# Kernel optimization log

Hardware: AMD Instinct MI355X
Metric: run time of the kernel (lower is better)

The kernel has to match this reference:

```python
import jax, jax.numpy as jnp
import numpy as np

TOPK = 7  # hard-coded k in cal_high_score_instance_mask
EPS_DICE = 1e-8


def setup_inputs() -> dict:
    key = jax.random.key(0)
    k1, k2, k3, k4 = jax.random.split(key, 4)
    b, n, v, h, w = 4, 16, 32, 160, 160
    pred_mask = jax.random.normal(k1, (b, 1, h, w), dtype=jnp.float32)
    encode_feat = jax.random.normal(k2, (b, v, h, w), dtype=jnp.float32)
    gt_instances = (jax.random.uniform(k3, (b, n, h, w)) > 0.8).astype(jnp.float32)
    # validity mask over instance slots
    gt_index_mask = jax.random.randint(k4, (b, n), 0, 2).astype(jnp.int32)
    return {
        "pred_mask": pred_mask,
        "encode_feat": encode_feat,
        "gt_instances": gt_instances,
        "gt_index_mask": gt_index_mask,
    }


def reference(pred_mask, encode_feat, gt_instances, gt_index_mask):
    b, v, h, w = encode_feat.shape
    n = gt_instances.shape[1]
    hw = h * w
    feat = encode_feat.reshape(b, v, hw)          # b, v, hw
    gt = gt_instances.reshape(b, n, hw)           # b, n, hw
    valid = gt_index_mask.astype(feat.dtype)      # b, n  (0/1)

    # ---- get_mean_embedding_vector: masked mean of embedding per instance
    pix = jnp.clip(gt.sum(-1), 1.0)               # b, n
    mean_emb = jnp.einsum('bvp,bnp->bnv', feat, gt) / pix[..., None]

    # ---- cal_high_score_instance_mask: topk over masked score map, gather embeddings
    pre_regions = pred_mask.reshape(b, 1, hw) * gt             # b, n, hw
    _wvals, idx = jax.lax.top_k(pre_regions, TOPK)              # b, n, k
    idx_flat = idx.reshape(b, n * TOPK)                         # b, n*k
    # gather embedding vectors at topk pixel locations -> b, n*k, v
    idx_feat_th = jnp.take_along_axis(feat, idx_flat[:, None, :], axis=2)
    idx_feat_th = jnp.transpose(idx_feat_th, (0, 2, 1))

    # ---- get_isntance_mask: embedding-vector x feature-map matmuls
    inst_masks = jnp.einsum('bkv,bvp->bkp', idx_feat_th, feat)  # b, n*k, hw
    mean_masks = jnp.einsum('bnv,bvp->bnp', mean_emb, feat)     # b, n, hw

    # ---- w_dice_loss on mean-embedding masks (valid instances only)
    p_mean = jax.nn.sigmoid(mean_masks)
    denom_mean = jnp.clip((p_mean ** 2).sum(-1) + (gt ** 2).sum(-1), EPS_DICE)
    dice_mean = 1.0 - 2.0 * (gt * p_mean).sum(-1) / denom_mean  # b, n
    mean_inst_loss = (dice_mean * valid).sum()

    # ---- w_dice_loss on topk-instance masks (target expanded over k)
    p_k = jax.nn.sigmoid(inst_masks.reshape(b, n, TOPK, hw))
    t_k = gt[:, :, None, :]                                     # b, n, 1, hw
    denom_k = jnp.clip((p_k ** 2).sum(-1) + (t_k ** 2).sum(-1), EPS_DICE)
    dice_k = 1.0 - 2.0 * (t_k * p_k).sum(-1) / denom_k          # b, n, k
    inst_loss = (dice_k * valid[..., None]).sum()

    # ---- l2_loss: masked squared distance of per-pixel embedding to instance mean
    diff = (feat[:, None, :, :] - mean_emb[..., None]) * gt[:, :, None, :]  # b, n, v, hw
    l2 = (diff ** 2).sum(-1) / pix[..., None]                   # b, n, v
    embedding_l2_loss = (l2.sum(-1) * valid).sum()

    return jnp.stack([mean_inst_loss, inst_loss, embedding_l2_loss])
```

## Files before the change

### kernel.cpp

```cpp
#include <hip/hip_runtime.h>
#include <cstdint>
#include <cstddef>

#define B 4
#define N 16
#define V 32
#define HW 25600
#define TOPK 7
#define NSLB 5
#define NCA 200
#define NCC 400

__device__ __forceinline__ bool better(float av, int ai, float bv, int bi) {
    return (av > bv) || (av == bv && ai < bi);
}


__device__ __forceinline__ void kTop_body(
    int slab, int tid,
    const float* __restrict__ pred, const float* __restrict__ gt,
    float* __restrict__ cand_val, int* __restrict__ cand_idx,
    float* __restrict__ cnt_part,
    float* rwv, int* rwi, float* csum) {
    int bn = slab / NSLB, sl = slab % NSLB;
    int b = bn >> 4;
    int lane = tid & 63, wave = tid >> 6;
    int base = sl * 5120;

    const float* gtrow = gt + (size_t)bn * HW + base;
    const float* pr = pred + (size_t)b * HW + base;

    float tv[TOPK]; int ti[TOPK];
#pragma unroll
    for (int j = 0; j < TOPK; ++j) { tv[j] = -INFINITY; ti[j] = 0x7fffffff; }
    float cnt = 0.f;

#pragma unroll
    for (int it = 0; it < 5; ++it) {
        int p = it * 1024 + tid * 4;
        float4 g4 = *reinterpret_cast<const float4*>(gtrow + p);
        float4 p4 = *reinterpret_cast<const float4*>(pr + p);
        cnt += g4.x + g4.y + g4.z + g4.w;
        float ca[4] = { p4.x * g4.x, p4.y * g4.y, p4.z * g4.z, p4.w * g4.w };
#pragma unroll
        for (int j = 0; j < 4; ++j) {
            float c = ca[j]; int pi = base + p + j;
            if (better(c, pi, tv[TOPK - 1], ti[TOPK - 1])) {
                tv[TOPK - 1] = c; ti[TOPK - 1] = pi;
#pragma unroll
                for (int q = TOPK - 2; q >= 0; --q) {
                    if (better(tv[q + 1], ti[q + 1], tv[q], ti[q])) {
                        float fv = tv[q]; int fi = ti[q];
                        tv[q] = tv[q + 1]; ti[q] = ti[q + 1];
                        tv[q + 1] = fv; ti[q + 1] = fi;
                    }
                }
            }
        }
    }

#pragma unroll
    for (int off = 32; off > 0; off >>= 1) cnt += __shfl_down(cnt, off);
    if (lane == 0) csum[wave] = cnt;
    __syncthreads();
    if (tid == 0) cnt_part[slab] = csum[0] + csum[1] + csum[2] + csum[3];

    int cbase = slab * TOPK;
    for (int r = 0; r < TOPK; ++r) {
        float bv = tv[0]; int bi = ti[0];
#pragma unroll
        for (int m = 1; m <= 32; m <<= 1) {
            float ov = __shfl_xor(bv, m);
            int oi = __shfl_xor(bi, m);
            if (better(ov, oi, bv, bi)) { bv = ov; bi = oi; }
        }
        if (lane == 0) { rwv[wave] = bv; rwi[wave] = bi; }
        __syncthreads();
        float fv = rwv[0]; int fi = rwi[0];
#pragma unroll
        for (int w = 1; w < 4; ++w)
            if (better(rwv[w], rwi[w], fv, fi)) { fv = rwv[w]; fi = rwi[w]; }
        if (ti[0] == fi) {
#pragma unroll
            for (int q = 0; q < TOPK - 1; ++q) { tv[q] = tv[q + 1]; ti[q] = ti[q + 1]; }
            tv[TOPK - 1] = -INFINITY; ti[TOPK - 1] = 0x7fffffff;
        }
        if (tid == 0) { cand_val[cbase + r] = fv; cand_idx[cbase + r] = fi; }
        __syncthreads();
    }
}

__device__ __forceinline__ void kA_body(
    int w, int tid,
    const float* __restrict__ feat, const float* __restrict__ gt,
    float* __restrict__ ms_part, float* __restrict__ s2_part) {
    int xcd = w & 7;
    int b = xcd >> 1;
    int ch = (w >> 3) * 2 + (xcd & 1);
    int c0 = ch * 128;
    int ng = tid >> 6, vg = (tid >> 3) & 7, pg = tid & 7;

    const float* gb = gt + (size_t)(b * N + ng * 4) * HW + c0 + pg * 4;
    const float* fb = feat + (size_t)(b * V + vg * 4) * HW + c0 + pg * 4;

    float acc[4][4];
#pragma unroll
    for (int i = 0; i < 4; ++i)
#pragma unroll
        for (int j = 0; j < 4; ++j) acc[i][j] = 0.f;
    float s2a[4] = { 0.f, 0.f, 0.f, 0.f };

#pragma unroll
    for (int q = 0; q < 4; ++q) {
        int p = q * 32;
        float4 g4[4], f4[4];
#pragma unroll
        for (int i = 0; i < 4; ++i)
            g4[i] = *reinterpret_cast<const float4*>(gb + (size_t)i * HW + p);
#pragma unroll
        for (int j = 0; j < 4; ++j)
            f4[j] = *reinterpret_cast<const float4*>(fb + (size_t)j * HW + p);
        float ffx = 0.f, ffy = 0.f, ffz = 0.f, ffw = 0.f;
#pragma unroll
        for (int j = 0; j < 4; ++j) {
            ffx = fmaf(f4[j].x, f4[j].x, ffx);
            ffy = fmaf(f4[j].y, f4[j].y, ffy);
            ffz = fmaf(f4[j].z, f4[j].z, ffz);
            ffw = fmaf(f4[j].w, f4[j].w, ffw);
        }
#pragma unroll
        for (int i = 0; i < 4; ++i) {
#pragma unroll
            for (int j = 0; j < 4; ++j) {
                acc[i][j] = fmaf(g4[i].x, f4[j].x, acc[i][j]);
                acc[i][j] = fmaf(g4[i].y, f4[j].y, acc[i][j]);
                acc[i][j] = fmaf(g4[i].z, f4[j].z, acc[i][j]);
                acc[i][j] = fmaf(g4[i].w, f4[j].w, acc[i][j]);
            }
            s2a[i] = fmaf(g4[i].x, ffx, s2a[i]);
            s2a[i] = fmaf(g4[i].y, ffy, s2a[i]);
            s2a[i] = fmaf(g4[i].z, ffz, s2a[i]);
            s2a[i] = fmaf(g4[i].w, ffw, s2a[i]);
        }
    }
#pragma unroll
    for (int m = 1; m <= 4; m <<= 1)
#pragma unroll
        for (int i = 0; i < 4; ++i)
#pragma unroll
            for (int j = 0; j < 4; ++j) acc[i][j] += __shfl_xor(acc[i][j], m);
    size_t blk = (size_t)(b * NCA + ch);
    if (pg == 0) {
        float* dst = ms_part + blk * 512;
#pragma unroll
        for (int i = 0; i < 4; ++i)
#pragma unroll
            for (int j = 0; j < 4; ++j)
                dst[(ng * 4 + i) * 32 + vg * 4 + j] = acc[i][j];
    }
#pragma unroll
    for (int m = 1; m <= 32; m <<= 1)
#pragma unroll
        for (int i = 0; i < 4; ++i) s2a[i] += __shfl_xor(s2a[i], m);
    if ((tid & 63) == 0) {
#pragma unroll
        for (int i = 0; i < 4; ++i)
            s2_part[blk * 16 + ng * 4 + i] = s2a[i];
    }
}

__global__ __launch_bounds__(256) void kAT(
    const float* __restrict__ pred, const float* __restrict__ feat,
    const float* __restrict__ gt,
    float* __restrict__ ms_part, float* __restrict__ s2_part,
    float* __restrict__ cand_val, int* __restrict__ cand_idx,
    float* __restrict__ cnt_part, float* __restrict__ out) {
    __shared__ float rwv[4]; __shared__ int rwi[4]; __shared__ float csum[4];
    int s = blockIdx.x;
    int tid = threadIdx.x;
    if (s == 0 && tid == 0) { out[0] = 0.f; out[1] = 0.f; out[2] = 0.f; }
    if (s < 800) kA_body(s, tid, feat, gt, ms_part, s2_part);
    else kTop_body(s - 800, tid, pred, gt, cand_val, cand_idx, cnt_part,
                   rwv, rwi, csum);
}

__global__ __launch_bounds__(256) void kB(
    const float* __restrict__ feat, const float* __restrict__ ms_part,
    const float* __restrict__ s2_part,
    const float* __restrict__ cand_val, const int* __restrict__ cand_idx,
    const float* __restrict__ cnt_part, const int* __restrict__ valid,
    float* __restrict__ Ebuf, float* __restrict__ cntbuf, float* __restrict__ out) {
    int bn = blockIdx.x;
    int b = bn >> 4, n = bn & 15;
    int tid = threadIdx.x;
    int lane = tid & 63, wave = tid >> 6;

    __shared__ float msl[8][33];
    __shared__ float s2w[4];
    __shared__ int idx7[TOPK];

    {
        int sl = tid >> 5, v = tid & 31;
        const float* src = ms_part + ((size_t)(b * NCA) + sl) * 512 + n * 32 + v;
        float sm = 0.f;
#pragma unroll 5
        for (int k = 0; k < 25; ++k) sm += src[(size_t)(8 * k) * 512];
        msl[sl][v] = sm;
    }
    {
        float s2v = 0.f;
        if (tid < NCA) s2v = s2_part[((size_t)(b * NCA) + tid) * 16 + n];
#pragma unroll
        for (int m = 1; m <= 32; m <<= 1) s2v += __shfl_xor(s2v, m);
        if (lane == 0) s2w[wave] = s2v;
    }
    if (wave == 0) {
        float cv = -INFINITY; int ci = 0x7fffffff;
        if (lane < NSLB * TOPK) {
            cv = cand_val[(size_t)bn * NSLB * TOPK + lane];
            ci = cand_idx[(size_t)bn * NSLB * TOPK + lane];
        }
#pragma unroll
        for (int r = 0; r < TOPK; ++r) {
            float bv = cv; int bi = ci;
#pragma unroll
            for (int m = 1; m <= 32; m <<= 1) {
                float ov = __shfl_xor(bv, m);
                int oi = __shfl_xor(bi, m);
                if (better(ov, oi, bv, bi)) { bv = ov; bi = oi; }
            }
            if (ci == bi) { cv = -INFINITY; ci = 0x7fffffff; }
            if (lane == 0) idx7[r] = bi;
        }
    }
    __syncthreads();

    if (tid < 32) {
        const float* cp = cnt_part + bn * NSLB;
        float cnt = cp[0] + cp[1] + cp[2] + cp[3] + cp[4];
        float msum = msl[0][tid] + msl[1][tid] + msl[2][tid] + msl[3][tid]
                   + msl[4][tid] + msl[5][tid] + msl[6][tid] + msl[7][tid];
        float pix = fmaxf(cnt, 1.0f);
        float mu = msum / pix;
        Ebuf[(size_t)bn * 256 + tid] = mu;
        float msq = mu * mu;
#pragma unroll
        for (int m = 1; m <= 16; m <<= 1) msq += __shfl_xor(msq, m);
        if (tid == 0) {
            cntbuf[bn] = cnt;
            float s2 = s2w[0] + s2w[1] + s2w[2] + s2w[3];
            atomicAdd(out + 2, (s2 / pix - msq) * (float)valid[bn]);
        }
    } else {
        int t = tid - 32;
        if (t < 224) {
            int r = t >> 5, v = t & 31;
            Ebuf[(size_t)bn * 256 + (r + 1) * 32 + v] =
                feat[((size_t)b * V + v) * HW + idx7[r]];
        }
    }
}

__global__ __launch_bounds__(256) void kC(
    const float* __restrict__ feat, const float* __restrict__ gt,
    const float* __restrict__ Ebuf, float* __restrict__ sums_part) {
    int s = blockIdx.x;
    int xcd = s & 7;
    int b = xcd >> 1;
    int ch = (s >> 3) * 2 + (xcd & 1);
    int c0 = ch * 64;
    int tid = threadIdx.x;
    int n = tid >> 4, pg = tid & 15;

    __shared__ __attribute__((aligned(16))) float f_lds[32][64];
    __shared__ float e_lds[8 * 16 * 36];
    __shared__ float red[16][17];

    const float* eb = Ebuf + (size_t)b * 4096;
#pragma unroll
    for (int k = 0; k < 4; ++k) {
        int q = (tid + 256 * k) * 4;
        int nn = q >> 8, rr = (q >> 5) & 7, vv = q & 31;
        *reinterpret_cast<float4*>(&e_lds[(rr * 16 + nn) * 36 + vv]) =
            *reinterpret_cast<const float4*>(eb + q);
    }
    {
        const float* fb0 = feat + (size_t)b * V * HW + c0;
#pragma unroll
        for (int k = 0; k < 2; ++k) {
            int u = tid + 256 * k;
            int v = u >> 4, p4 = (u & 15) * 4;
            *reinterpret_cast<float4*>(&f_lds[v][p4]) =
                *reinterpret_cast<const float4*>(fb0 + (size_t)v * HW + p4);
        }
    }
    __syncthreads();

    float4 g4 = *reinterpret_cast<const float4*>(gt + (size_t)(b * N + n) * HW + c0 + pg * 4);

    float acc[8][4];
#pragma unroll
    for (int r = 0; r < 8; ++r)
#pragma unroll
        for (int j = 0; j < 4; ++j) acc[r][j] = 0.f;

#pragma unroll
    for (int vq = 0; vq < 8; ++vq) {
        float4 f0 = *reinterpret_cast<const float4*>(&f_lds[vq * 4 + 0][pg * 4]);
        float4 f1 = *reinterpret_cast<const float4*>(&f_lds[vq * 4 + 1][pg * 4]);
        float4 f2 = *reinterpret_cast<const float4*>(&f_lds[vq * 4 + 2][pg * 4]);
        float4 f3 = *reinterpret_cast<const float4*>(&f_lds[vq * 4 + 3][pg * 4]);
#pragma unroll
        for (int r = 0; r < 8; ++r) {
            float4 e4 = *reinterpret_cast<const float4*>(&e_lds[(r * 16 + n) * 36 + vq * 4]);
            acc[r][0] = fmaf(e4.x, f0.x, acc[r][0]);
            acc[r][0] = fmaf(e4.y, f1.x, acc[r][0]);
            acc[r][0] = fmaf(e4.z, f2.x, acc[r][0]);
            acc[r][0] = fmaf(e4.w, f3.x, acc[r][0]);
            acc[r][1] = fmaf(e4.x, f0.y, acc[r][1]);
            acc[r][1] = fmaf(e4.y, f1.y, acc[r][1]);
            acc[r][1] = fmaf(e4.z, f2.y, acc[r][1]);
            acc[r][1] = fmaf(e4.w, f3.y, acc[r][1]);
            acc[r][2] = fmaf(e4.x, f0.z, acc[r][2]);
            acc[r][2] = fmaf(e4.y, f1.z, acc[r][2]);
            acc[r][2] = fmaf(e4.z, f2.z, acc[r][2]);
            acc[r][2] = fmaf(e4.w, f3.z, acc[r][2]);
            acc[r][3] = fmaf(e4.x, f0.w, acc[r][3]);
            acc[r][3] = fmaf(e4.y, f1.w, acc[r][3]);
            acc[r][3] = fmaf(e4.z, f2.w, acc[r][3]);
            acc[r][3] = fmaf(e4.w, f3.w, acc[r][3]);
        }
    }

    float p2[8], tp[8];
#pragma unroll
    for (int r = 0; r < 8; ++r) { p2[r] = 0.f; tp[r] = 0.f; }
    float ga[4] = { g4.x, g4.y, g4.z, g4.w };
#pragma unroll
    for (int r = 0; r < 8; ++r)
#pragma unroll
        for (int j = 0; j < 4; ++j) {
            float sg = 1.f / (1.f + __expf(-acc[r][j]));
            p2[r] = fmaf(sg, sg, p2[r]);
            tp[r] = fmaf(ga[j], sg, tp[r]);
        }
#pragma unroll
    for (int m = 1; m <= 8; m <<= 1)
#pragma unroll
        for (int r = 0; r < 8; ++r) {
            p2[r] += __shfl_xor(p2[r], m);
            tp[r] += __shfl_xor(tp[r], m);
        }
    if (pg == 0) {
#pragma unroll
        for (int r = 0; r < 8; ++r) {
            red[n][r * 2] = p2[r];
            red[n][r * 2 + 1] = tp[r];
        }
    }
    __syncthreads();
    sums_part[(size_t)(b * NCC + ch) * 256 + tid] = red[tid >> 4][tid & 15];
}

__global__ __launch_bounds__(256) void kD(
    const float* __restrict__ sums_part, const float* __restrict__ cntbuf,
    const int* __restrict__ valid, float* __restrict__ out) {
    int bn = blockIdx.x;
    int b = bn >> 4, n = bn & 15;
    int tid = threadIdx.x;
    int slot = tid & 15, cg = tid >> 4;
    int lane = tid & 63, wave = tid >> 6;

    __shared__ float red2[4][17];
    __shared__ float fin[16];

    float sv = 0.f;
    const float* src = sums_part + (size_t)b * NCC * 256 + n * 16 + slot;
    for (int k = 0; k < 25; ++k) sv += src[(size_t)(cg + 16 * k) * 256];
    sv += __shfl_xor(sv, 16);
    sv += __shfl_xor(sv, 32);
    if (lane < 16) red2[wave][lane] = sv;
    __syncthreads();
    if (tid < 16) fin[tid] = red2[0][tid] + red2[1][tid] + red2[2][tid] + red2[3][tid];
    __syncthreads();

    if (tid == 0) {
        float vw = (float)valid[bn];
        float cnt = cntbuf[bn];
        float mloss = 0.f, iloss = 0.f;
#pragma unroll
        for (int r = 0; r < 8; ++r) {
            float p2 = fin[r * 2];
            float tp = fin[r * 2 + 1];
            float denom = fmaxf(p2 + cnt, 1e-8f);
            float dice = 1.f - 2.f * tp / denom;
            if (r == 0) mloss = dice * vw;
            else iloss += dice * vw;
        }
        atomicAdd(out + 0, mloss);
        atomicAdd(out + 1, iloss);
    }
}

extern "C" void kernel_launch(void* const* d_in, const int* in_sizes, int n_in,
                              void* d_out, int out_size, void* d_ws, size_t ws_size,
                              hipStream_t stream) {
    const float* pred = (const float*)d_in[0];
    const float* feat = (const float*)d_in[1];
    const float* gtin = (const float*)d_in[2];
    const int* valid  = (const int*)d_in[3];
    float* out = (float*)d_out;

    char* ws = (char*)d_ws;
    float* ms_part   = (float*)(ws);
    float* s2_part   = (float*)(ws + 1638400);
    float* cand_val  = (float*)(ws + 1689600);
    int*   cand_idx  = (int*)  (ws + 1698560);
    float* cnt_part  = (float*)(ws + 1707520);
    float* sums_part = (float*)(ws + 1708800);
    float* Ebuf      = (float*)(ws + 3347200);
    float* cntbuf    = (float*)(ws + 3412736);

    kAT<<<800 + B * N * NSLB, 256, 0, stream>>>(pred, feat, gtin, ms_part, s2_part,
                                                cand_val, cand_idx, cnt_part, out);
    kB<<<B * N, 256, 0, stream>>>(feat, ms_part, s2_part, cand_val, cand_idx,
                                  cnt_part, valid, Ebuf, cntbuf, out);
    kC<<<B * NCC, 256, 0, stream>>>(feat, gtin, Ebuf, sums_part);
    kD<<<B * N, 256, 0, stream>>>(sums_part, cntbuf, valid, out);
}
```

Before: 60.23 us.

## Stage gt tile in LDS for kA and fuse final reduction via last-block counter

Two changes. In kA, the gt tile is loaded once into shared memory and each thread reads its rows from there. Before, every thread fetched 4 gt rows straight from global memory, and threads with different vg read the same data again. Separately, kD is removed and its reduction is folded into kC through an atomic per-batch completion counter. The last block of each batch sums all partials and does the dice/atomic output, which saves one kernel launch but makes that final reduction serial in a single block.

```diff
diff --git a/kernel.cpp b/kernel.cpp
--- a/kernel.cpp
+++ b/kernel.cpp
@@ -93,14 +93,26 @@
 __device__ __forceinline__ void kA_body(
     int w, int tid,
     const float* __restrict__ feat, const float* __restrict__ gt,
-    float* __restrict__ ms_part, float* __restrict__ s2_part) {
+    float* __restrict__ ms_part, float* __restrict__ s2_part,
+    float (*g_lds)[132]) {
     int xcd = w & 7;
     int b = xcd >> 1;
     int ch = (w >> 3) * 2 + (xcd & 1);
     int c0 = ch * 128;
     int ng = tid >> 6, vg = (tid >> 3) & 7, pg = tid & 7;
 
-    const float* gb = gt + (size_t)(b * N + ng * 4) * HW + c0 + pg * 4;
+    {
+        const float* gb0 = gt + (size_t)(b * N) * HW + c0;
+#pragma unroll
+        for (int k = 0; k < 2; ++k) {
+            int u = tid + 256 * k;
+            int row = u >> 5, p4 = (u & 31) * 4;
+            *reinterpret_cast<float4*>(&g_lds[row][p4]) =
+                *reinterpret_cast<const float4*>(gb0 + (size_t)row * HW + p4);
+        }
+    }
+    __syncthreads();
+
     const float* fb = feat + (size_t)(b * V + vg * 4) * HW + c0 + pg * 4;
 
     float acc[4][4];
@@ -112,14 +124,14 @@
 
 #pragma unroll
     for (int q = 0; q < 4; ++q) {
-        int p = q * 32;
+        int p = q * 32 + pg * 4;
         float4 g4[4], f4[4];
 #pragma unroll
         for (int i = 0; i < 4; ++i)
-            g4[i] = *reinterpret_cast<const float4*>(gb + (size_t)i * HW + p);
+            g4[i] = *reinterpret_cast<const float4*>(&g_lds[ng * 4 + i][p]);
 #pragma unroll
         for (int j = 0; j < 4; ++j)
-            f4[j] = *reinterpret_cast<const float4*>(fb + (size_t)j * HW + p);
+            f4[j] = *reinterpret_cast<const float4*>(fb + (size_t)j * HW + q * 32);
         float ffx = 0.f, ffy = 0.f, ffz = 0.f, ffw = 0.f;
 #pragma unroll
         for (int j = 0; j < 4; ++j) {
@@ -174,12 +186,17 @@
     const float* __restrict__ gt,
     float* __restrict__ ms_part, float* __restrict__ s2_part,
     float* __restrict__ cand_val, int* __restrict__ cand_idx,
-    float* __restrict__ cnt_part, float* __restrict__ out) {
+    float* __restrict__ cnt_part, float* __restrict__ out,
+    int* __restrict__ done_cnt) {
+    __shared__ float g_lds[16][132];
     __shared__ float rwv[4]; __shared__ int rwi[4]; __shared__ float csum[4];
     int s = blockIdx.x;
     int tid = threadIdx.x;
-    if (s == 0 && tid == 0) { out[0] = 0.f; out[1] = 0.f; out[2] = 0.f; }
-    if (s < 800) kA_body(s, tid, feat, gt, ms_part, s2_part);
+    if (s == 0) {
+        if (tid == 0) { out[0] = 0.f; out[1] = 0.f; out[2] = 0.f; }
+        if (tid < 4) done_cnt[tid] = 0;
+    }
+    if (s < 800) kA_body(s, tid, feat, gt, ms_part, s2_part, g_lds);
     else kTop_body(s - 800, tid, pred, gt, cand_val, cand_idx, cnt_part,
                    rwv, rwi, csum);
 }
@@ -261,9 +278,11 @@
     }
 }
 
-__global__ __launch_bounds__(256) void kC(
+__global__ __launch_bounds__(256) void kCD(
     const float* __restrict__ feat, const float* __restrict__ gt,
-    const float* __restrict__ Ebuf, float* __restrict__ sums_part) {
+    const float* __restrict__ Ebuf, float* __restrict__ sums_part,
+    const float* __restrict__ cntbuf, const int* __restrict__ valid,
+    float* __restrict__ out, int* __restrict__ done_cnt) {
     int s = blockIdx.x;
     int xcd = s & 7;
     int b = xcd >> 1;
@@ -275,6 +294,8 @@
     __shared__ __attribute__((aligned(16))) float f_lds[32][64];
     __shared__ float e_lds[8 * 16 * 36];
     __shared__ float red[16][17];
+    __shared__ int lastflag;
+    __shared__ float fin2[16][17];
 
     const float* eb = Ebuf + (size_t)b * 4096;
 #pragma unroll
@@ -360,40 +381,36 @@
     }
     __syncthreads();
     sums_part[(size_t)(b * NCC + ch) * 256 + tid] = red[tid >> 4][tid & 15];
-}
-
-__global__ __launch_bounds__(256) void kD(
-    const float* __restrict__ sums_part, const float* __restrict__ cntbuf,
-    const int* __restrict__ valid, float* __restrict__ out) {
-    int bn = blockIdx.x;
-    int b = bn >> 4, n = bn & 15;
-    int tid = threadIdx.x;
-    int slot = tid & 15, cg = tid >> 4;
-    int lane = tid & 63, wave = tid >> 6;
-
-    __shared__ float red2[4][17];
-    __shared__ float fin[16];
-
-    float sv = 0.f;
-    const float* src = sums_part + (size_t)b * NCC * 256 + n * 16 + slot;
-    for (int k = 0; k < 25; ++k) sv += src[(size_t)(cg + 16 * k) * 256];
-    sv += __shfl_xor(sv, 16);
-    sv += __shfl_xor(sv, 32);
-    if (lane < 16) red2[wave][lane] = sv;
-    __syncthreads();
-    if (tid < 16) fin[tid] = red2[0][tid] + red2[1][tid] + red2[2][tid] + red2[3][tid];
-    __syncthreads();
-
+
+    __threadfence();
     if (tid == 0) {
+        int old = atomicAdd(&done_cnt[b], 1);
+        lastflag = (old == NCC - 1);
+    }
+    __syncthreads();
+    if (!lastflag) return;
+    __threadfence();
+
+    {
+        int slot = tid & 15;
+        float sv = 0.f;
+        const float* src = sums_part + (size_t)b * NCC * 256 + n * 16 + slot;
+#pragma unroll 8
+        for (int k = 0; k < NCC; ++k) sv += src[(size_t)k * 256];
+        fin2[n][slot] = sv;
+    }
+    __syncthreads();
+    if (tid < 16) {
+        int bn = b * 16 + tid;
         float vw = (float)valid[bn];
         float cnt = cntbuf[bn];
         float mloss = 0.f, iloss = 0.f;
 #pragma unroll
         for (int r = 0; r < 8; ++r) {
-            float p2 = fin[r * 2];
-            float tp = fin[r * 2 + 1];
-            float denom = fmaxf(p2 + cnt, 1e-8f);
-            float dice = 1.f - 2.f * tp / denom;
+            float pp = fin2[tid][r * 2];
+            float tt = fin2[tid][r * 2 + 1];
+            float denom = fmaxf(pp + cnt, 1e-8f);
+            float dice = 1.f - 2.f * tt / denom;
             if (r == 0) mloss = dice * vw;
             else iloss += dice * vw;
         }
@@ -420,11 +437,13 @@
     float* sums_part = (float*)(ws + 1708800);
     float* Ebuf      = (float*)(ws + 3347200);
     float* cntbuf    = (float*)(ws + 3412736);
+    int*   done_cnt  = (int*)  (ws + 3412992);
 
     kAT<<<800 + B * N * NSLB, 256, 0, stream>>>(pred, feat, gtin, ms_part, s2_part,
-                                                cand_val, cand_idx, cnt_part, out);
+                                                cand_val, cand_idx, cnt_part, out,
+                                                done_cnt);
     kB<<<B * N, 256, 0, stream>>>(feat, ms_part, s2_part, cand_val, cand_idx,
                                   cnt_part, valid, Ebuf, cntbuf, out);
-    kC<<<B * NCC, 256, 0, stream>>>(feat, gtin, Ebuf, sums_part);
-    kD<<<B * N, 256, 0, stream>>>(sums_part, cntbuf, valid, out);
-}
+    kCD<<<B * NCC, 256, 0, stream>>>(feat, gtin, Ebuf, sums_part, cntbuf, valid,
+                                     out, done_cnt);
+}
```

New measurement: 172.0 us. 186% more time.
